# Kernel optimization log

Measured on AMD Instinct MI355X. Metric: run time of the kernel, lower is better.

Reference implementation:

```python
import jax, jax.numpy as jnp
import numpy as np

EPS = 1e-5  # torch GroupNorm default eps


def _pairwise_sqdist(x, y):
    # squared euclidean distance matrix, clamped at 0 for numerical safety
    d = (jnp.sum(x * x, -1)[:, None] + jnp.sum(y * y, -1)[None, :]
         - 2.0 * (x @ y.T))
    return jnp.maximum(d, 0.0)


def _pc_normalize(ref, src):
    # jointly center and scale both clouds to the unit sphere
    pts = jnp.concatenate([ref, src], axis=0)
    centroid = pts.mean(axis=0, keepdims=True)
    pts = pts - centroid
    m = jnp.max(jnp.linalg.norm(pts, axis=1))
    pts = pts / m
    n_ref = ref.shape[0]
    return pts[:n_ref], pts[n_ref:]


def _group_norm(x, gamma, beta, groups):
    N, C = x.shape
    xg = x.reshape(N, groups, C // groups)
    mean = xg.mean(-1, keepdims=True)
    var = jnp.mean((xg - mean) ** 2, -1, keepdims=True)
    xn = ((xg - mean) / jnp.sqrt(var + EPS)).reshape(N, C)
    return xn * gamma + beta


def setup_inputs() -> dict:
    key = jax.random.key(0)
    ks = jax.random.split(key, 8)
    N_ref, N_src, D = 128, 128, 256
    points_c = jax.random.normal(ks[0], (N_ref + N_src, 3), jnp.float32)
    ref_feats = jax.random.normal(ks[1], (N_ref, D), jnp.float32)
    src_feats = jax.random.normal(ks[2], (N_src, D), jnp.float32)
    # normalized features, as the '_norm' names suggest
    ref_feats = ref_feats / jnp.linalg.norm(ref_feats, axis=-1, keepdims=True)
    src_feats = src_feats / jnp.linalg.norm(src_feats, axis=-1, keepdims=True)
    # a valid rigid transform: random rotation + small translation
    A = jax.random.normal(ks[3], (3, 3), jnp.float32)
    Q, _ = jnp.linalg.qr(A)
    trans = jnp.eye(4, dtype=jnp.float32)
    trans = trans.at[:3, :3].set(Q)
    trans = trans.at[:3, 3].set(jax.random.normal(ks[4], (3,), jnp.float32) * 0.1)
    s = 1.0 / np.sqrt(512)
    return {
        'points_c': points_c,
        'ref_feats_c_norm': ref_feats,
        'src_feats_c_norm': src_feats,
        'trans': trans,
        'W1': jax.random.normal(ks[5], (256, 512), jnp.float32) * s,
        'b1': jnp.zeros((256,), jnp.float32),
        'g1': jnp.ones((256,), jnp.float32),
        'bt1': jnp.zeros((256,), jnp.float32),
        'W2': jax.random.normal(ks[6], (128, 256), jnp.float32) * (1.0 / np.sqrt(256)),
        'b2': jnp.zeros((128,), jnp.float32),
        'g2': jnp.ones((128,), jnp.float32),
        'bt2': jnp.zeros((128,), jnp.float32),
        'W3': jax.random.normal(ks[7], (2, 128), jnp.float32) * (1.0 / np.sqrt(128)),
        'b3': jnp.zeros((2,), jnp.float32),
        'ref_length': 128,
    }


def reference(points_c, ref_feats_c_norm, src_feats_c_norm, trans,
              W1, b1, g1, bt1, W2, b2, g2, bt2, W3, b3, ref_length):
    GROUPS = 8
    ref_points = points_c[:ref_length]
    src_points = points_c[ref_length:]
    # apply rigid transform to src points
    src_points = src_points @ trans[:3, :3].T + trans[:3, 3]
    ref_n, src_n = _pc_normalize(ref_points, src_points)

    dist_mat = jnp.exp(-_pairwise_sqdist(ref_n, src_n))  # [Nr, Ns]
    match_idx_ref = jnp.argmax(dist_mat, axis=1)
    match_idx_src = jnp.argmax(dist_mat, axis=0)
    min_dist_ref = jnp.max(dist_mat, axis=1)
    min_dist_src = jnp.max(dist_mat, axis=0)

    feat_score_mat = ref_feats_c_norm @ src_feats_c_norm.T  # [Nr, Ns]
    feat_match_idx_ref = jnp.argmax(feat_score_mat, axis=1)
    feat_match_idx_src = jnp.argmax(feat_score_mat, axis=0)
    feat_match_ref = jnp.max(feat_score_mat, axis=1)
    feat_match_src = jnp.max(feat_score_mat, axis=0)

    r_idx = jnp.arange(feat_score_mat.shape[0])
    c_idx = jnp.arange(feat_score_mat.shape[1])
    feat_score_ref = feat_score_mat[r_idx, match_idx_ref]
    feat_score_src = feat_score_mat[match_idx_src, c_idx]
    dist_ref = dist_mat[r_idx, feat_match_idx_ref]
    dist_src = dist_mat[feat_match_idx_src, c_idx]

    min_dist = jnp.concatenate([min_dist_ref, min_dist_src])
    feat_score = jnp.concatenate([feat_score_ref, feat_score_src])
    perm_d = jnp.argsort(-min_dist)  # descending sort
    d_m = min_dist[perm_d] * feat_score[perm_d]

    match_feat = jnp.concatenate([feat_match_ref, feat_match_src])
    match_dist = jnp.concatenate([dist_ref, dist_src])
    perm_f = jnp.argsort(-match_feat)
    m_d = match_dist[perm_f] * match_feat[perm_f]

    geo_out = jnp.concatenate([d_m, m_d])[None, :]  # [1, 512]

    h = _group_norm(geo_out @ W1.T + b1, g1, bt1, GROUPS)
    h = jax.nn.relu(h)
    h = _group_norm(h @ W2.T + b2, g2, bt2, GROUPS)
    h = jax.nn.relu(h)
    return h @ W3.T + b3  # [1, num_classes]
```

## Files before the change

### kernel.cpp

```cpp
#include <hip/hip_runtime.h>
#include <math.h>

#define NREF 128
#define NSRC 128
#define DIM  256
#define EPS  1e-5f

__global__ __launch_bounds__(512) void side_kernel(
    const float* __restrict__ points_c,
    const float* __restrict__ trans,
    const float* __restrict__ ref_feats,
    const float* __restrict__ src_feats,
    float* __restrict__ arrs)
{
    __shared__ float px[256], py[256], pz[256], nsq[256];
    __shared__ float wred[12];
    __shared__ float red[4];
    __shared__ float featLds[128];
    __shared__ float cvD[8]; __shared__ int ciD[8];
    __shared__ float cvF[8]; __shared__ int ciF[8];

    const int b = blockIdx.x;
    const int t = threadIdx.x;
    const int w = t >> 6, l = t & 63;

    const bool isRow = (b < NREF);
    const int  me    = isRow ? b : (b - NREF);

    float x = 0.f, y = 0.f, z = 0.f;
    if (t < 256) {
        x = points_c[3 * t + 0];
        y = points_c[3 * t + 1];
        z = points_c[3 * t + 2];
        if (t >= NREF) {
            float nx = trans[0] * x + trans[1] * y + trans[2]  * z + trans[3];
            float ny = trans[4] * x + trans[5] * y + trans[6]  * z + trans[7];
            float nz = trans[8] * x + trans[9] * y + trans[10] * z + trans[11];
            x = nx; y = ny; z = nz;
        }
    }

    const float* __restrict__ myrow = (isRow ? ref_feats : src_feats) + me * DIM;
    const float4* __restrict__ other = (const float4*)(isRow ? src_feats : ref_feats);
    const float4 r = ((const float4*)myrow)[l];

    float bfv = -2.f; int bfi = 0;
    for (int m = 0; m < 16; m += 2) {
        const int j0 = w * 16 + m, j1 = j0 + 1;
        const float4 a0 = other[j0 * 64 + l];
        const float4 a1 = other[j1 * 64 + l];
        float acc0 = a0.x * r.x + a0.y * r.y + a0.z * r.z + a0.w * r.w;
        float acc1 = a1.x * r.x + a1.y * r.y + a1.z * r.z + a1.w * r.w;
        for (int off = 32; off >= 1; off >>= 1) {
            acc0 += __shfl_xor(acc0, off);
            acc1 += __shfl_xor(acc1, off);
        }
        if (l == 0) { featLds[j0] = acc0; featLds[j1] = acc1; }
        if (acc0 > bfv) { bfv = acc0; bfi = j0; }
        if (acc1 > bfv) { bfv = acc1; bfi = j1; }
    }
    if (l == 0) { cvF[w] = bfv; ciF[w] = bfi; }

    if (t < 256) {
        float sx = x, sy = y, sz = z;
        for (int off = 32; off >= 1; off >>= 1) {
            sx += __shfl_down(sx, off);
            sy += __shfl_down(sy, off);
            sz += __shfl_down(sz, off);
        }
        if (l == 0) { wred[w] = sx; wred[4 + w] = sy; wred[8 + w] = sz; }
    }
    __syncthreads();
    if (t == 0) {
        red[0] = (wred[0] + wred[1] + wred[2] + wred[3]) * (1.0f / 256.0f);
        red[1] = (wred[4] + wred[5] + wred[6] + wred[7]) * (1.0f / 256.0f);
        red[2] = (wred[8] + wred[9] + wred[10] + wred[11]) * (1.0f / 256.0f);
    }
    __syncthreads();
    if (t < 256) {
        x -= red[0]; y -= red[1]; z -= red[2];
        float n = x * x + y * y + z * z;
        float mx = n;
        for (int off = 32; off >= 1; off >>= 1)
            mx = fmaxf(mx, __shfl_down(mx, off));
        if (l == 0) wred[w] = mx;
    }
    __syncthreads();
    if (t == 0)
        red[3] = 1.0f / sqrtf(fmaxf(fmaxf(wred[0], wred[1]), fmaxf(wred[2], wred[3])));
    __syncthreads();
    if (t < 256) {
        const float inv = red[3];
        x *= inv; y *= inv; z *= inv;
        px[t] = x; py[t] = y; pz[t] = z;
        nsq[t] = x * x + y * y + z * z;
    }
    __syncthreads();

    float bdv = -1.f; int bdi = 0;
    for (int m = 0; m < 16; ++m) {
        const int jj = w * 16 + m;
        const int i = isRow ? me : jj;
        const int j = isRow ? jj : me;
        float d = nsq[i] + nsq[128 + j]
                - 2.0f * (px[i] * px[128 + j] + py[i] * py[128 + j] + pz[i] * pz[128 + j]);
        d = fmaxf(d, 0.f);
        const float v = expf(-d);
        if (v > bdv) { bdv = v; bdi = jj; }
    }
    if (l == 0) { cvD[w] = bdv; ciD[w] = bdi; }
    __syncthreads();

    if (t == 0) {
        float bv = -1.f; int bi = 0;
        for (int q = 0; q < 8; ++q)
            if (cvD[q] > bv) { bv = cvD[q]; bi = ciD[q]; }
        float fv = -2.f; int fi = 0;
        for (int q = 0; q < 8; ++q)
            if (cvF[q] > fv) { fv = cvF[q]; fi = ciF[q]; }
        const float fscore = featLds[bi];
        const int i = isRow ? me : fi;
        const int j = isRow ? fi : me;
        float d = nsq[i] + nsq[128 + j]
                - 2.0f * (px[i] * px[128 + j] + py[i] * py[128 + j] + pz[i] * pz[128 + j]);
        d = fmaxf(d, 0.f);
        const float mdist = expf(-d);
        const int gi = isRow ? me : NREF + me;
        arrs[gi]       = bv;
        arrs[256 + gi] = fscore;
        arrs[512 + gi] = fv;
        arrs[768 + gi] = mdist;
    }
}

__global__ __launch_bounds__(512) void tail_kernel(
    const float* __restrict__ arrs,
    const float* __restrict__ W1, const float* __restrict__ b1,
    const float* __restrict__ g1, const float* __restrict__ bt1,
    const float* __restrict__ W2, const float* __restrict__ b2,
    const float* __restrict__ g2, const float* __restrict__ bt2,
    const float* __restrict__ W3, const float* __restrict__ b3,
    float* __restrict__ out)
{
    __shared__ __align__(16) float arrD[256], arrFS[256], arrMF[256], arrMD[256];
    __shared__ __align__(16) float geoLds[512];
    __shared__ __align__(16) float h1s[256];
    __shared__ float y1s[256];
    __shared__ float stats[16];
    __shared__ float y2s[128], h2s[128];

    const int t = threadIdx.x;
    const int w = t >> 6, l = t & 63;

    if (t < 256) {
        arrD[t]  = arrs[t];
        arrFS[t] = arrs[256 + t];
        arrMF[t] = arrs[512 + t];
        arrMD[t] = arrs[768 + t];
    }
    __syncthreads();

    {
        const int e = t & 255;
        const float* __restrict__ A = (t < 256) ? arrD : arrMF;
        const float v = A[e];
        int rk = 0;
        for (int jb = 0; jb < 256; jb += 4) {
            const float4 u = ((const float4*)A)[jb >> 2];
            rk += (u.x > v) || (u.x == v && (jb + 0) < e);
            rk += (u.y > v) || (u.y == v && (jb + 1) < e);
            rk += (u.z > v) || (u.z == v && (jb + 2) < e);
            rk += (u.w > v) || (u.w == v && (jb + 3) < e);
        }
        if (t < 256) geoLds[rk]       = arrD[e] * arrFS[e];
        else         geoLds[256 + rk] = arrMD[e] * arrMF[e];
    }
    __syncthreads();

    {
        const float4 ga = ((const float4*)geoLds)[l];
        const float4 gb = ((const float4*)geoLds)[64 + l];
        for (int m = 0; m < 32; ++m) {
            const int c = (w << 5) + m;
            const float4* __restrict__ wrow = (const float4*)(W1 + c * 512);
            const float4 a = wrow[l];
            const float4 bq = wrow[64 + l];
            float acc = a.x * ga.x + a.y * ga.y + a.z * ga.z + a.w * ga.w
                      + bq.x * gb.x + bq.y * gb.y + bq.z * gb.z + bq.w * gb.w;
            acc += __shfl_down(acc, 32);
            acc += __shfl_down(acc, 16);
            acc += __shfl_down(acc, 8);
            acc += __shfl_down(acc, 4);
            acc += __shfl_down(acc, 2);
            acc += __shfl_down(acc, 1);
            if (l == 0) y1s[c] = acc + b1[c];
        }
    }
    __syncthreads();

    if (t < 8) {
        float s = 0.f;
        for (int k = 0; k < 32; ++k) s += y1s[(t << 5) + k];
        const float mean = s * (1.0f / 32.0f);
        float q = 0.f;
        for (int k = 0; k < 32; ++k) { const float d = y1s[(t << 5) + k] - mean; q += d * d; }
        stats[t] = mean;
        stats[8 + t] = rsqrtf(q * (1.0f / 32.0f) + EPS);
    }
    __syncthreads();
    if (t < 256) {
        const int g = t >> 5;
        const float xn = (y1s[t] - stats[g]) * stats[8 + g];
        h1s[t] = fmaxf(xn * g1[t] + bt1[t], 0.f);
    }
    __syncthreads();

    {
        const float4 hv = ((const float4*)h1s)[l];
        for (int m = 0; m < 16; ++m) {
            const int c = (w << 4) + m;
            const float4 wv = ((const float4*)(W2 + c * 256))[l];
            float acc = wv.x * hv.x + wv.y * hv.y + wv.z * hv.z + wv.w * hv.w;
            acc += __shfl_down(acc, 32);
            acc += __shfl_down(acc, 16);
            acc += __shfl_down(acc, 8);
            acc += __shfl_down(acc, 4);
            acc += __shfl_down(acc, 2);
            acc += __shfl_down(acc, 1);
            if (l == 0) y2s[c] = acc + b2[c];
        }
    }
    __syncthreads();

    if (t < 128) {
        const int g = t >> 4;
        float s = 0.f;
        for (int k = 0; k < 16; ++k) s += y2s[(g << 4) + k];
        const float mean = s * (1.0f / 16.0f);
        float q = 0.f;
        for (int k = 0; k < 16; ++k) { const float d = y2s[(g << 4) + k] - mean; q += d * d; }
        const float xn = (y2s[t] - mean) * rsqrtf(q * (1.0f / 16.0f) + EPS);
        h2s[t] = fmaxf(xn * g2[t] + bt2[t], 0.f);
    }
    __syncthreads();
    if (t < 128) {
        float acc = W3[w * 128 + l] * h2s[l]
                  + W3[w * 128 + 64 + l] * h2s[64 + l];
        acc += __shfl_down(acc, 32);
        acc += __shfl_down(acc, 16);
        acc += __shfl_down(acc, 8);
        acc += __shfl_down(acc, 4);
        acc += __shfl_down(acc, 2);
        acc += __shfl_down(acc, 1);
        if (l == 0) out[w] = acc + b3[w];
    }
}

extern "C" void kernel_launch(void* const* d_in, const int* in_sizes, int n_in,
                              void* d_out, int out_size, void* d_ws, size_t ws_size,
                              hipStream_t stream)
{
    const float* points_c  = (const float*)d_in[0];
    const float* ref_feats = (const float*)d_in[1];
    const float* src_feats = (const float*)d_in[2];
    const float* trans     = (const float*)d_in[3];
    const float* W1  = (const float*)d_in[4];
    const float* b1  = (const float*)d_in[5];
    const float* g1  = (const float*)d_in[6];
    const float* bt1 = (const float*)d_in[7];
    const float* W2  = (const float*)d_in[8];
    const float* b2  = (const float*)d_in[9];
    const float* g2  = (const float*)d_in[10];
    const float* bt2 = (const float*)d_in[11];
    const float* W3  = (const float*)d_in[12];
    const float* b3  = (const float*)d_in[13];

    float* arrs = (float*)d_ws;

    side_kernel<<<dim3(256), dim3(512), 0, stream>>>(points_c, trans, ref_feats, src_feats, arrs);
    tail_kernel<<<dim3(1), dim3(512), 0, stream>>>(arrs, W1, b1, g1, bt1,
                                                   W2, b2, g2, bt2, W3, b3,
                                                   (float*)d_out);
}
```

Baseline: 129.1 us.

## Split single-block MLP tail into multi-block per-layer kernels

Replaces the single-block tail kernel with three kernels. The first uses 256 blocks, each redoing the rank sort and computing one W1 output row. The second uses 128 blocks for group norm plus W2, and the third is a one-block final layer. The aim is to spread the serial weight-streaming GEMVs across many compute units instead of one. The cost is two extra kernel launches, and every block in the first kernel recomputes the sort.

New measurement: 104.3 us. -19.2%, faster.

```diff
diff --git a/kernel.cpp b/kernel.cpp
--- a/kernel.cpp
+++ b/kernel.cpp
@@ -133,127 +133,138 @@
     }
 }
 
-__global__ __launch_bounds__(512) void tail_kernel(
+__global__ __launch_bounds__(256) void mlp1_kernel(
     const float* __restrict__ arrs,
     const float* __restrict__ W1, const float* __restrict__ b1,
+    float* __restrict__ y1)
+{
+    __shared__ __align__(16) float arrD[256], arrFS[256], arrMF[256], arrMD[256];
+    __shared__ __align__(16) float geoLds[512];
+    const int c = blockIdx.x;
+    const int t = threadIdx.x;
+
+    arrD[t]  = arrs[t];
+    arrFS[t] = arrs[256 + t];
+    arrMF[t] = arrs[512 + t];
+    arrMD[t] = arrs[768 + t];
+    __syncthreads();
+
+    {
+        const float vD = arrD[t];
+        const float vF = arrMF[t];
+        int rD = 0, rF = 0;
+        for (int jb = 0; jb < 64; ++jb) {
+            const float4 uD = ((const float4*)arrD)[jb];
+            const float4 uF = ((const float4*)arrMF)[jb];
+            const int j0 = 4 * jb;
+            rD += (uD.x > vD) || (uD.x == vD && (j0 + 0) < t);
+            rD += (uD.y > vD) || (uD.y == vD && (j0 + 1) < t);
+            rD += (uD.z > vD) || (uD.z == vD && (j0 + 2) < t);
+            rD += (uD.w > vD) || (uD.w == vD && (j0 + 3) < t);
+            rF += (uF.x > vF) || (uF.x == vF && (j0 + 0) < t);
+            rF += (uF.y > vF) || (uF.y == vF && (j0 + 1) < t);
+            rF += (uF.z > vF) || (uF.z == vF && (j0 + 2) < t);
+            rF += (uF.w > vF) || (uF.w == vF && (j0 + 3) < t);
+        }
+        geoLds[rD]       = vD * arrFS[t];
+        geoLds[256 + rF] = arrMD[t] * vF;
+    }
+    __syncthreads();
+
+    if (t < 64) {
+        const int l = t;
+        const float4 ga = ((const float4*)geoLds)[l];
+        const float4 gb = ((const float4*)geoLds)[64 + l];
+        const float4* __restrict__ wrow = (const float4*)(W1 + c * 512);
+        const float4 a = wrow[l];
+        const float4 b = wrow[64 + l];
+        float acc = a.x * ga.x + a.y * ga.y + a.z * ga.z + a.w * ga.w
+                  + b.x * gb.x + b.y * gb.y + b.z * gb.z + b.w * gb.w;
+        acc += __shfl_down(acc, 32);
+        acc += __shfl_down(acc, 16);
+        acc += __shfl_down(acc, 8);
+        acc += __shfl_down(acc, 4);
+        acc += __shfl_down(acc, 2);
+        acc += __shfl_down(acc, 1);
+        if (l == 0) y1[c] = acc + b1[c];
+    }
+}
+
+__global__ __launch_bounds__(64) void mlp2_kernel(
+    const float* __restrict__ y1,
     const float* __restrict__ g1, const float* __restrict__ bt1,
     const float* __restrict__ W2, const float* __restrict__ b2,
+    float* __restrict__ y2)
+{
+    __shared__ __align__(16) float y1s[256];
+    __shared__ float stats[16];
+    const int c = blockIdx.x, l = threadIdx.x;
+    ((float4*)y1s)[l] = ((const float4*)y1)[l];
+    __syncthreads();
+    if (l < 8) {
+        float s = 0.f;
+        for (int k = 0; k < 32; ++k) s += y1s[(l << 5) + k];
+        const float mean = s * (1.0f / 32.0f);
+        float q = 0.f;
+        for (int k = 0; k < 32; ++k) { const float d = y1s[(l << 5) + k] - mean; q += d * d; }
+        const float var = q * (1.0f / 32.0f);
+        stats[l] = mean;
+        stats[8 + l] = rsqrtf(var + EPS);
+    }
+    __syncthreads();
+    const float4 gg = ((const float4*)g1)[l];
+    const float4 bb = ((const float4*)bt1)[l];
+    const int g = l >> 3;
+    const float mean = stats[g], inv = stats[8 + g];
+    const float4 yv = ((const float4*)y1s)[l];
+    float4 h;
+    h.x = fmaxf((yv.x - mean) * inv * gg.x + bb.x, 0.f);
+    h.y = fmaxf((yv.y - mean) * inv * gg.y + bb.y, 0.f);
+    h.z = fmaxf((yv.z - mean) * inv * gg.z + bb.z, 0.f);
+    h.w = fmaxf((yv.w - mean) * inv * gg.w + bb.w, 0.f);
+    const float4 wv = ((const float4*)(W2 + c * 256))[l];
+    float acc = wv.x * h.x + wv.y * h.y + wv.z * h.z + wv.w * h.w;
+    acc += __shfl_down(acc, 32);
+    acc += __shfl_down(acc, 16);
+    acc += __shfl_down(acc, 8);
+    acc += __shfl_down(acc, 4);
+    acc += __shfl_down(acc, 2);
+    acc += __shfl_down(acc, 1);
+    if (l == 0) y2[c] = acc + b2[c];
+}
+
+__global__ __launch_bounds__(128) void final_kernel(
+    const float* __restrict__ y2,
     const float* __restrict__ g2, const float* __restrict__ bt2,
     const float* __restrict__ W3, const float* __restrict__ b3,
     float* __restrict__ out)
 {
-    __shared__ __align__(16) float arrD[256], arrFS[256], arrMF[256], arrMD[256];
-    __shared__ __align__(16) float geoLds[512];
-    __shared__ __align__(16) float h1s[256];
-    __shared__ float y1s[256];
-    __shared__ float stats[16];
-    __shared__ float y2s[128], h2s[128];
-
+    __shared__ float y2s[128], h2[128];
     const int t = threadIdx.x;
-    const int w = t >> 6, l = t & 63;
-
-    if (t < 256) {
-        arrD[t]  = arrs[t];
-        arrFS[t] = arrs[256 + t];
-        arrMF[t] = arrs[512 + t];
-        arrMD[t] = arrs[768 + t];
-    }
-    __syncthreads();
-
+    y2s[t] = y2[t];
+    __syncthreads();
     {
-        const int e = t & 255;
-        const float* __restrict__ A = (t < 256) ? arrD : arrMF;
-        const float v = A[e];
-        int rk = 0;
-        for (int jb = 0; jb < 256; jb += 4) {
-            const float4 u = ((const float4*)A)[jb >> 2];
-            rk += (u.x > v) || (u.x == v && (jb + 0) < e);
-            rk += (u.y > v) || (u.y == v && (jb + 1) < e);
-            rk += (u.z > v) || (u.z == v && (jb + 2) < e);
-            rk += (u.w > v) || (u.w == v && (jb + 3) < e);
-        }
-        if (t < 256) geoLds[rk]       = arrD[e] * arrFS[e];
-        else         geoLds[256 + rk] = arrMD[e] * arrMF[e];
-    }
-    __syncthreads();
-
-    {
-        const float4 ga = ((const float4*)geoLds)[l];
-        const float4 gb = ((const float4*)geoLds)[64 + l];
-        for (int m = 0; m < 32; ++m) {
-            const int c = (w << 5) + m;
-            const float4* __restrict__ wrow = (const float4*)(W1 + c * 512);
-            const float4 a = wrow[l];
-            const float4 bq = wrow[64 + l];
-            float acc = a.x * ga.x + a.y * ga.y + a.z * ga.z + a.w * ga.w
-                      + bq.x * gb.x + bq.y * gb.y + bq.z * gb.z + bq.w * gb.w;
-            acc += __shfl_down(acc, 32);
-            acc += __shfl_down(acc, 16);
-            acc += __shfl_down(acc, 8);
-            acc += __shfl_down(acc, 4);
-            acc += __shfl_down(acc, 2);
-            acc += __shfl_down(acc, 1);
-            if (l == 0) y1s[c] = acc + b1[c];
-        }
-    }
-    __syncthreads();
-
-    if (t < 8) {
-        float s = 0.f;
-        for (int k = 0; k < 32; ++k) s += y1s[(t << 5) + k];
-        const float mean = s * (1.0f / 32.0f);
-        float q = 0.f;
-        for (int k = 0; k < 32; ++k) { const float d = y1s[(t << 5) + k] - mean; q += d * d; }
-        stats[t] = mean;
-        stats[8 + t] = rsqrtf(q * (1.0f / 32.0f) + EPS);
-    }
-    __syncthreads();
-    if (t < 256) {
-        const int g = t >> 5;
-        const float xn = (y1s[t] - stats[g]) * stats[8 + g];
-        h1s[t] = fmaxf(xn * g1[t] + bt1[t], 0.f);
-    }
-    __syncthreads();
-
-    {
-        const float4 hv = ((const float4*)h1s)[l];
-        for (int m = 0; m < 16; ++m) {
-            const int c = (w << 4) + m;
-            const float4 wv = ((const float4*)(W2 + c * 256))[l];
-            float acc = wv.x * hv.x + wv.y * hv.y + wv.z * hv.z + wv.w * hv.w;
-            acc += __shfl_down(acc, 32);
-            acc += __shfl_down(acc, 16);
-            acc += __shfl_down(acc, 8);
-            acc += __shfl_down(acc, 4);
-            acc += __shfl_down(acc, 2);
-            acc += __shfl_down(acc, 1);
-            if (l == 0) y2s[c] = acc + b2[c];
-        }
-    }
-    __syncthreads();
-
-    if (t < 128) {
         const int g = t >> 4;
         float s = 0.f;
         for (int k = 0; k < 16; ++k) s += y2s[(g << 4) + k];
         const float mean = s * (1.0f / 16.0f);
         float q = 0.f;
         for (int k = 0; k < 16; ++k) { const float d = y2s[(g << 4) + k] - mean; q += d * d; }
-        const float xn = (y2s[t] - mean) * rsqrtf(q * (1.0f / 16.0f) + EPS);
-        h2s[t] = fmaxf(xn * g2[t] + bt2[t], 0.f);
-    }
-    __syncthreads();
-    if (t < 128) {
-        float acc = W3[w * 128 + l] * h2s[l]
-                  + W3[w * 128 + 64 + l] * h2s[64 + l];
-        acc += __shfl_down(acc, 32);
-        acc += __shfl_down(acc, 16);
-        acc += __shfl_down(acc, 8);
-        acc += __shfl_down(acc, 4);
-        acc += __shfl_down(acc, 2);
-        acc += __shfl_down(acc, 1);
-        if (l == 0) out[w] = acc + b3[w];
-    }
+        const float var = q * (1.0f / 16.0f);
+        const float xn = (y2s[t] - mean) * rsqrtf(var + EPS);
+        h2[t] = fmaxf(xn * g2[t] + bt2[t], 0.f);
+    }
+    __syncthreads();
+    const int wave = t >> 6, lane = t & 63;
+    float acc = W3[wave * 128 + lane] * h2[lane]
+              + W3[wave * 128 + 64 + lane] * h2[64 + lane];
+    acc += __shfl_down(acc, 32);
+    acc += __shfl_down(acc, 16);
+    acc += __shfl_down(acc, 8);
+    acc += __shfl_down(acc, 4);
+    acc += __shfl_down(acc, 2);
+    acc += __shfl_down(acc, 1);
+    if (lane == 0) out[wave] = acc + b3[wave];
 }
 
 extern "C" void kernel_launch(void* const* d_in, const int* in_sizes, int n_in,
@@ -276,9 +287,11 @@
     const float* b3  = (const float*)d_in[13];
 
     float* arrs = (float*)d_ws;
+    float* y1   = arrs + 1024;
+    float* y2   = arrs + 1280;
 
     side_kernel<<<dim3(256), dim3(512), 0, stream>>>(points_c, trans, ref_feats, src_feats, arrs);
-    tail_kernel<<<dim3(1), dim3(512), 0, stream>>>(arrs, W1, b1, g1, bt1,
-                                                   W2, b2, g2, bt2, W3, b3,
-                                                   (float*)d_out);
-}
+    mlp1_kernel<<<dim3(256), dim3(256), 0, stream>>>(arrs, W1, b1, y1);
+    mlp2_kernel<<<dim3(128), dim3(64), 0, stream>>>(y1, g1, bt1, W2, b2, y2);
+    final_kernel<<<dim3(1), dim3(128), 0, stream>>>(y2, g2, bt2, W3, b3, (float*)d_out);
+}
```
